# Kernel optimization log

Measured on AMD Instinct MI355X. Metric: run time of the kernel, lower is better.

The kernel has to match this reference:

```python
import jax, jax.numpy as jnp
import numpy as np

C = 512       # out_channels
RATIO = 2
K = C // RATIO          # init_channels = 256
NEW = K * (RATIO - 1)   # new_channels = 256
H = W = 160
EPS = 1e-5


def _conv(x, w, pad, groups=1):
    return jax.lax.conv_general_dilated(
        x, w, (1, 1), [(pad, pad), (pad, pad)],
        dimension_numbers=("NCHW", "OIHW", "NCHW"),
        feature_group_count=groups)


def _bn(x, g, b, m, v):
    scale = (g / jnp.sqrt(v + EPS))[None, :, None, None]
    return (x - m[None, :, None, None]) * scale + b[None, :, None, None]


def setup_inputs() -> dict:
    key = jax.random.key(0)
    ks = jax.random.split(key, 16)
    s = 0.05
    return {
        "x": jax.random.normal(ks[0], (1, C, H, W), jnp.float32),
        "w_fc1": jax.random.normal(ks[1], (K, C), jnp.float32) * s,
        "w_fc2": jax.random.normal(ks[2], (C, K), jnp.float32) * s,
        "w_cheap": jax.random.normal(ks[3], (NEW, 1, 3, 3), jnp.float32) * s,  # depthwise, groups=K
        "bn1_g": jnp.ones((NEW,), jnp.float32),
        "bn1_b": jnp.zeros((NEW,), jnp.float32),
        "bn1_m": jax.random.normal(ks[4], (NEW,), jnp.float32) * s,
        "bn1_v": jax.random.uniform(ks[5], (NEW,), jnp.float32, 0.5, 1.5),
        "w_dc1": jax.random.normal(ks[6], (C, 2 * C, 1, 1), jnp.float32) * s,
        "b_dc1": jax.random.normal(ks[7], (C,), jnp.float32) * s,
        "bn2_g": jnp.ones((C,), jnp.float32),
        "bn2_b": jnp.zeros((C,), jnp.float32),
        "bn2_m": jax.random.normal(ks[8], (C,), jnp.float32) * s,
        "bn2_v": jax.random.uniform(ks[9], (C,), jnp.float32, 0.5, 1.5),
        "w_dc2": jax.random.normal(ks[10], (C, C, 3, 3), jnp.float32) * s,
        "b_dc2": jax.random.normal(ks[11], (C,), jnp.float32) * s,
    }


def reference(x, w_fc1, w_fc2, w_cheap, bn1_g, bn1_b, bn1_m, bn1_v,
              w_dc1, b_dc1, bn2_g, bn2_b, bn2_m, bn2_v, w_dc2, b_dc2):
    # ---- channel attention (CBAM-style shared MLP over avg+max pool) ----
    avg = x.mean(axis=(2, 3))                      # [1, C]
    mx = x.max(axis=(2, 3))                        # [1, C]
    mlp = lambda p: jax.nn.relu(p @ w_fc1.T) @ w_fc2.T
    scales = jax.nn.sigmoid(mlp(avg) + mlp(mx))    # [1, C]
    # ---- sort-based top-K channel select, kept in channel-index order ----
    # torch: sort desc, drop channels ranked >= K via boolean mask (mask is in
    # channel-index order), equivalent to gathering sorted top-K indices.
    _, top_idx = jax.lax.top_k(scales[0], K)
    idx = jnp.sort(top_idx)
    x1 = x[:, idx]                                 # [1, K, H, W]
    # ---- cheap operation: depthwise 3x3 + BN + ReLU ----
    x2 = jax.nn.relu(_bn(_conv(x1, w_cheap, 1, groups=K), bn1_g, bn1_b, bn1_m, bn1_v))
    # ---- concat [x*scales, x1, x2] -> 2C channels ----
    cat = jnp.concatenate([x * scales[:, :, None, None], x1, x2], axis=1)
    # ---- down_channel: 1x1 conv + BN + 3x3 conv + ReLU ----
    h = _conv(cat, w_dc1, 0) + b_dc1[None, :, None, None]
    h = _bn(h, bn2_g, bn2_b, bn2_m, bn2_v)
    h = _conv(h, w_dc2, 1) + b_dc2[None, :, None, None]
    return jax.nn.relu(h)
```

## Files before the change

kernel.cpp:

```cpp
#include <hip/hip_runtime.h>
#include <math.h>

#define C 512
#define K 256
#define HW 160
#define NPIX (HW*HW)
#define PW 162
#define EPS 1e-5f

typedef __attribute__((ext_vector_type(8))) short s16x8;
typedef __attribute__((ext_vector_type(16))) float f32x16;

__device__ __forceinline__ unsigned short f2bf(float f) {
    unsigned int u = __float_as_uint(f);
    u += 0x7fffu + ((u >> 16) & 1u);
    return (unsigned short)(u >> 16);
}

__device__ __forceinline__ void ldg_lds16(const void* g, void* l) {
    __builtin_amdgcn_global_load_lds((const __attribute__((address_space(1))) unsigned int*)g,
                                     (__attribute__((address_space(3))) unsigned int*)l, 16, 0, 0);
}

#define WAIT_VM0()   asm volatile("s_waitcnt vmcnt(0)" ::: "memory")
#define WAIT_VM14()  asm volatile("s_waitcnt vmcnt(14)" ::: "memory")
#define WAIT_VM23()  asm volatile("s_waitcnt vmcnt(23)" ::: "memory")

__global__ void reduce_kernel(const float* __restrict__ x,
                              float* __restrict__ avg, float* __restrict__ mx) {
    int c = blockIdx.x;
    const float4* xc = (const float4*)(x + (size_t)c * NPIX);
    float s = 0.f, m = -INFINITY;
    for (int p = threadIdx.x; p < NPIX / 4; p += 256) {
        float4 v = xc[p];
        s += v.x + v.y + v.z + v.w;
        m = fmaxf(m, fmaxf(fmaxf(v.x, v.y), fmaxf(v.z, v.w)));
    }
    __shared__ float ss[256], sm[256];
    ss[threadIdx.x] = s; sm[threadIdx.x] = m;
    __syncthreads();
    for (int o = 128; o > 0; o >>= 1) {
        if (threadIdx.x < o) {
            ss[threadIdx.x] += ss[threadIdx.x + o];
            sm[threadIdx.x] = fmaxf(sm[threadIdx.x], sm[threadIdx.x + o]);
        }
        __syncthreads();
    }
    if (threadIdx.x == 0) {
        avg[c] = ss[0] / (float)NPIX;
        mx[c]  = sm[0];
    }
}

__global__ void mlp_select_kernel(const float* __restrict__ avg,
                                  const float* __restrict__ mx,
                                  const float* __restrict__ w_fc1,
                                  const float* __restrict__ w_fc2,
                                  float* __restrict__ scales_out,
                                  int* __restrict__ idx,
                                  int* __restrict__ pos) {
    __shared__ float s_avg[C], s_mx[C], s_h[K], s_scales[C];
    __shared__ int s_sel[C];
    int t = threadIdx.x;
    s_avg[t] = avg[t];
    s_mx[t]  = mx[t];
    __syncthreads();
    if (t < K) {
        float ha = 0.f, hm = 0.f;
        const float4* wr = (const float4*)(w_fc1 + (size_t)t * C);
        for (int c = 0; c < C / 4; c++) {
            float4 w = wr[c];
            ha += s_avg[4*c]*w.x + s_avg[4*c+1]*w.y + s_avg[4*c+2]*w.z + s_avg[4*c+3]*w.w;
            hm += s_mx[4*c]*w.x + s_mx[4*c+1]*w.y + s_mx[4*c+2]*w.z + s_mx[4*c+3]*w.w;
        }
        s_h[t] = fmaxf(ha, 0.f) + fmaxf(hm, 0.f);
    }
    __syncthreads();
    {
        float o = 0.f;
        const float4* wr = (const float4*)(w_fc2 + (size_t)t * K);
        for (int k = 0; k < K / 4; k++) {
            float4 w = wr[k];
            o += s_h[4*k]*w.x + s_h[4*k+1]*w.y + s_h[4*k+2]*w.z + s_h[4*k+3]*w.w;
        }
        float sc = 1.f / (1.f + expf(-o));
        s_scales[t] = sc;
        scales_out[t] = sc;
    }
    __syncthreads();
    {
        float v = s_scales[t];
        int rank = 0;
        for (int i = 0; i < C; i++) {
            float u = s_scales[i];
            rank += (u > v) || (u == v && i < t);
        }
        s_sel[t] = (rank < K) ? 1 : 0;
    }
    __syncthreads();
    {
        int p = 0;
        for (int i = 0; i < t; i++) p += s_sel[i];
        if (s_sel[t]) { idx[p] = t; pos[t] = p; }
        else pos[t] = -1;
    }
}

__global__ void prep_kernel(const float* __restrict__ w_dc2, unsigned short* __restrict__ w3,
                            const float* __restrict__ w_dc1, const float* __restrict__ scales,
                            const int* __restrict__ pos, unsigned short* __restrict__ wA,
                            unsigned short* __restrict__ hpad,
                            const float* __restrict__ b_dc1,
                            const float* __restrict__ g2, const float* __restrict__ b2,
                            const float* __restrict__ m2, const float* __restrict__ v2,
                            float* __restrict__ scale2, float* __restrict__ shift2) {
    __shared__ unsigned short lw[4608];
    int b = blockIdx.x;
    if (b < 512) {
        int co = b;
        const float* src = w_dc2 + (size_t)co * 4608;
        for (int u = threadIdx.x; u < 4608; u += 256)
            lw[u] = f2bf(src[u]);
        __syncthreads();
        for (int u = threadIdx.x; u < 4608; u += 256) {
            int t = u >> 9, ci = u & 511;
            w3[((size_t)t * 512 + co) * 512 + ci] = lw[ci * 9 + t];
        }
    } else if (b < 1024) {
        int co = b - 512;
        const float* wr = w_dc1 + (size_t)co * 1024;
        for (int c = threadIdx.x; c < 768; c += 256) {
            float v;
            if (c < 512) {
                v = wr[c] * scales[c];
                int pp = pos[c];
                if (pp >= 0) v += wr[512 + pp];
            } else {
                v = wr[768 + (c - 512)];
            }
            wA[(size_t)co * 768 + c] = f2bf(v);
        }
    } else if (b < 1185) {
        int t = (b - 1024) * 256 + threadIdx.x;
        int pix = t >> 6;
        int p;
        if (pix < 162)      p = pix;
        else if (pix < 324) p = 161 * PW + (pix - 162);
        else {
            int r = pix - 324;
            p = (1 + (r >> 1)) * PW + ((r & 1) ? 161 : 0);
        }
        *(uint4*)&hpad[(size_t)p * 512 + (t & 63) * 8] = make_uint4(0u, 0u, 0u, 0u);
    } else {
        for (int c = threadIdx.x; c < C; c += 256) {
            float s = g2[c] * rsqrtf(v2[c] + EPS);
            scale2[c] = s;
            shift2[c] = (b_dc1[c] - m2[c]) * s + b2[c];
        }
    }
}

__global__ void dw_t_kernel(const float* __restrict__ x,
                            const int* __restrict__ idx,
                            const float* __restrict__ wch,
                            const float* __restrict__ g1, const float* __restrict__ b1,
                            const float* __restrict__ m1, const float* __restrict__ v1,
                            unsigned short* __restrict__ xcat) {
    __shared__ float tile[32][33];
    int tx = threadIdx.x & 31, ty = threadIdx.x >> 5;
    int pbase = blockIdx.x * 32, kbase = blockIdx.y * 32;
    int y = pbase / HW, x0 = pbase % HW;
    int px = x0 + tx;
#pragma unroll
    for (int jj = 0; jj < 4; jj++) {
        int k = kbase + ty + jj * 8;
        int c = idx[k];
        const float* xc = x + (size_t)c * NPIX;
        const float* wk = wch + k * 9;
        float acc = 0.f;
#pragma unroll
        for (int dy = 0; dy < 3; dy++) {
            int yy = y + dy - 1;
            if (yy < 0 || yy >= HW) continue;
#pragma unroll
            for (int dx = 0; dx < 3; dx++) {
                int xv = px + dx - 1;
                if (xv < 0 || xv >= HW) continue;
                acc += xc[yy * HW + xv] * wk[dy * 3 + dx];
            }
        }
        float s = g1[k] * rsqrtf(v1[k] + EPS);
        tile[ty + jj * 8][tx] = fmaxf((acc - m1[k]) * s + b1[k], 0.f);
    }
    __syncthreads();
#pragma unroll
    for (int jj = 0; jj < 4; jj++) {
        int p = pbase + ty + jj * 8;
        xcat[(size_t)p * 768 + 512 + kbase + tx] = f2bf(tile[tx][ty + jj * 8]);
    }
}

__global__ void transpose_kernel(const float* __restrict__ x,
                                 unsigned short* __restrict__ xcat) {
    __shared__ float tile[32][33];
    int tx = threadIdx.x & 31, ty = threadIdx.x >> 5;
    int pbase = blockIdx.x * 32, cbase = blockIdx.y * 32;
#pragma unroll
    for (int j = 0; j < 4; j++) {
        int c = cbase + ty + j * 8;
        tile[ty + j * 8][tx] = x[(size_t)c * NPIX + pbase + tx];
    }
    __syncthreads();
#pragma unroll
    for (int j = 0; j < 4; j++) {
        int p = pbase + ty + j * 8;
        xcat[(size_t)p * 768 + cbase + tx] = f2bf(tile[tx][ty + j * 8]);
    }
}

__global__ __launch_bounds__(64, 1) void conv1_mfma(const unsigned short* __restrict__ xcat,
        const unsigned short* __restrict__ wA,
        const float* __restrict__ scale2, const float* __restrict__ shift2,
        unsigned short* __restrict__ hpad) {
    __shared__ unsigned short Al[3][640 * 8];
    __shared__ unsigned short Bl[3][256 * 8];
    int y = blockIdx.x, co0 = blockIdx.y * 64;
    int lane = threadIdx.x;
    int l31 = lane & 31, q = lane >> 5;
    f32x16 acc[5][2] = {};

    int aoff[10], boff[4];
#pragma unroll
    for (int r = 0; r < 10; r++) {
        int g = r * 64 + lane;
        int px = g >> 2, jg = (g & 3) ^ ((px >> 1) & 3);
        aoff[r] = px * 768 + jg * 8;
    }
#pragma unroll
    for (int r = 0; r < 4; r++) {
        int g = r * 64 + lane;
        int co = g >> 2, jg = (g & 3) ^ ((co >> 1) & 3);
        boff[r] = co * 768 + jg * 8;
    }
    int raoff[2];
#pragma unroll
    for (int s = 0; s < 2; s++)
        raoff[s] = l31 * 64 + (((s * 2 + q) ^ ((l31 >> 1) & 3)) << 4);
    const unsigned short* arow = xcat + (size_t)y * HW * 768;
    const unsigned short* brow = wA + (size_t)co0 * 768;

    auto stage = [&](int ph, int buf) {
        int kc = ph * 32;
        unsigned short* An = Al[buf];
        unsigned short* Bn = Bl[buf];
#pragma unroll
        for (int r = 0; r < 10; r++) ldg_lds16(arow + kc + aoff[r], &An[r * 512]);
#pragma unroll
        for (int r = 0; r < 4; r++)  ldg_lds16(brow + kc + boff[r], &Bn[r * 512]);
    };

    stage(0, 0);
    stage(1, 1);
    for (int ph = 0; ph < 24; ph++) {
        const unsigned short* Ar = Al[ph % 3];
        const unsigned short* Br = Bl[ph % 3];
        if (ph == 23) { WAIT_VM0(); } else { WAIT_VM14(); }
#pragma unroll
        for (int s = 0; s < 2; s++) {
            s16x8 af[5], bf[2];
#pragma unroll
            for (int i = 0; i < 5; i++)
                af[i] = *(const s16x8*)((const char*)Ar + i * 2048 + raoff[s]);
#pragma unroll
            for (int j = 0; j < 2; j++)
                bf[j] = *(const s16x8*)((const char*)Br + j * 2048 + raoff[s]);
            if (s == 0 && ph < 22) stage(ph + 2, (ph + 2) % 3);
#pragma unroll
            for (int i = 0; i < 5; i++)
#pragma unroll
                for (int j = 0; j < 2; j++)
                    acc[i][j] = __builtin_amdgcn_mfma_f32_32x32x16_bf16(af[i], bf[j], acc[i][j], 0, 0, 0);
        }
    }
#pragma unroll
    for (int j = 0; j < 2; j++) {
        int co = co0 + j * 32 + l31;
        float s2 = scale2[co], sh = shift2[co];
#pragma unroll
        for (int i = 0; i < 5; i++) {
#pragma unroll
            for (int rg = 0; rg < 4; rg++) {
#pragma unroll
                for (int t = 0; t < 4; t++) {
                    int px = i * 32 + t + rg * 8 + q * 4;
                    size_t pp = (size_t)(y + 1) * PW + px + 1;
                    hpad[pp * 512 + co] = f2bf(acc[i][j][rg * 4 + t] * s2 + sh);
                }
            }
        }
    }
}

__global__ __launch_bounds__(64, 1) void conv3_mfma(const unsigned short* __restrict__ hpad,
        const unsigned short* __restrict__ w3,
        const float* __restrict__ bias, float* __restrict__ out) {
    __shared__ unsigned short Al[3][648 * 8];
    __shared__ unsigned short Bl[3][768 * 8];
    int y = blockIdx.x, co0 = blockIdx.y * 64;
    int lane = threadIdx.x;
    int l31 = lane & 31, q = lane >> 5;
    f32x16 acc[5][2] = {};

    int aoff[11], boff[12];
#pragma unroll
    for (int r = 0; r < 11; r++) {
        int g = r * 64 + lane;
        int px = g >> 2, jg = (g & 3) ^ ((px >> 1) & 3);
        aoff[r] = px * 512 + jg * 8;
    }
#pragma unroll
    for (int r = 0; r < 12; r++) {
        int g = r * 64 + lane;
        int tt = g >> 8, co = (g >> 2) & 63, jg = (g & 3) ^ ((co >> 1) & 3);
        boff[r] = (tt * 512 + co) * 512 + jg * 8;
    }
    int raoff[3][2], rboff[2];
#pragma unroll
    for (int dx = 0; dx < 3; dx++)
#pragma unroll
        for (int s = 0; s < 2; s++) {
            int m = l31 + dx;
            raoff[dx][s] = m * 64 + ((((s * 2 + q)) ^ ((m >> 1) & 3)) << 4);
        }
#pragma unroll
    for (int s = 0; s < 2; s++)
        rboff[s] = l31 * 64 + (((s * 2 + q) ^ ((l31 >> 1) & 3)) << 4);

    auto stage = [&](int ph, int buf) {
        int dy = ph >> 4, kc = (ph & 15) * 32;
        const unsigned short* ab = hpad + ((size_t)(y + dy) * PW) * 512 + kc;
        unsigned short* An = Al[buf];
#pragma unroll
        for (int r = 0; r < 10; r++) ldg_lds16(ab + aoff[r], &An[r * 512]);
        if (lane < 8)                ldg_lds16(ab + aoff[10], &An[10 * 512]);
        const unsigned short* bb = w3 + ((size_t)(dy * 3) * 512 + co0) * 512 + kc;
        unsigned short* Bn = Bl[buf];
#pragma unroll
        for (int r = 0; r < 12; r++) ldg_lds16(bb + boff[r], &Bn[r * 512]);
    };

    stage(0, 0);
    stage(1, 1);
    for (int ph = 0; ph < 48; ph++) {
        const unsigned short* Ar = Al[ph % 3];
        const unsigned short* Br = Bl[ph % 3];
        if (ph == 47) { WAIT_VM0(); } else { WAIT_VM23(); }
#pragma unroll
        for (int dx = 0; dx < 3; dx++) {
            s16x8 af[5][2], bf[2][2];
#pragma unroll
            for (int s = 0; s < 2; s++) {
#pragma unroll
                for (int i = 0; i < 5; i++)
                    af[i][s] = *(const s16x8*)((const char*)Ar + i * 2048 + raoff[dx][s]);
#pragma unroll
                for (int j = 0; j < 2; j++)
                    bf[j][s] = *(const s16x8*)((const char*)Br + dx * 4096 + j * 2048 + rboff[s]);
            }
            if (dx == 0 && ph < 46) stage(ph + 2, (ph + 2) % 3);
#pragma unroll
            for (int s = 0; s < 2; s++)
#pragma unroll
                for (int i = 0; i < 5; i++)
#pragma unroll
                    for (int j = 0; j < 2; j++)
                        acc[i][j] = __builtin_amdgcn_mfma_f32_32x32x16_bf16(af[i][s], bf[j][s], acc[i][j], 0, 0, 0);
        }
    }
#pragma unroll
    for (int j = 0; j < 2; j++) {
        int co = co0 + j * 32 + l31;
        float b = bias[co];
        float* op = out + (size_t)co * NPIX + y * HW;
#pragma unroll
        for (int i = 0; i < 5; i++) {
#pragma unroll
            for (int rg = 0; rg < 4; rg++) {
                int px = i * 32 + rg * 8 + q * 4;
                float4 v;
                v.x = fmaxf(acc[i][j][rg * 4 + 0] + b, 0.f);
                v.y = fmaxf(acc[i][j][rg * 4 + 1] + b, 0.f);
                v.z = fmaxf(acc[i][j][rg * 4 + 2] + b, 0.f);
                v.w = fmaxf(acc[i][j][rg * 4 + 3] + b, 0.f);
                *(float4*)&op[px] = v;
            }
        }
    }
}

extern "C" void kernel_launch(void* const* d_in, const int* in_sizes, int n_in,
                              void* d_out, int out_size, void* d_ws, size_t ws_size,
                              hipStream_t stream) {
    const float* x      = (const float*)d_in[0];
    const float* w_fc1  = (const float*)d_in[1];
    const float* w_fc2  = (const float*)d_in[2];
    const float* w_ch   = (const float*)d_in[3];
    const float* bn1_g  = (const float*)d_in[4];
    const float* bn1_b  = (const float*)d_in[5];
    const float* bn1_m  = (const float*)d_in[6];
    const float* bn1_v  = (const float*)d_in[7];
    const float* w_dc1  = (const float*)d_in[8];
    const float* b_dc1  = (const float*)d_in[9];
    const float* bn2_g  = (const float*)d_in[10];
    const float* bn2_b  = (const float*)d_in[11];
    const float* bn2_m  = (const float*)d_in[12];
    const float* bn2_v  = (const float*)d_in[13];
    const float* w_dc2  = (const float*)d_in[14];
    const float* b_dc2  = (const float*)d_in[15];
    float* out = (float*)d_out;

    char* ws = (char*)d_ws;
    float* avg    = (float*)(ws + 0);
    float* mx     = (float*)(ws + 2048);
    float* scales = (float*)(ws + 4096);
    int*   idx    = (int*)  (ws + 6144);
    int*   pos    = (int*)  (ws + 7168);
    float* scale2 = (float*)(ws + 9216);
    float* shift2 = (float*)(ws + 11264);
    unsigned short* wA   = (unsigned short*)(ws + 16384);
    unsigned short* w3   = (unsigned short*)(ws + 802816);
    unsigned short* xcat = (unsigned short*)(ws + 31735808);
    unsigned short* hpad = (unsigned short*)(ws + 71057408);

    reduce_kernel<<<C, 256, 0, stream>>>(x, avg, mx);
    mlp_select_kernel<<<1, C, 0, stream>>>(avg, mx, w_fc1, w_fc2, scales, idx, pos);
    prep_kernel<<<1186, 256, 0, stream>>>(w_dc2, w3, w_dc1, scales, pos, wA, hpad,
                                          b_dc1, bn2_g, bn2_b, bn2_m, bn2_v, scale2, shift2);
    dw_t_kernel<<<dim3(800, 8), 256, 0, stream>>>(x, idx, w_ch, bn1_g, bn1_b, bn1_m, bn1_v, xcat);
    transpose_kernel<<<dim3(800, 16), 256, 0, stream>>>(x, xcat);
    conv1_mfma<<<dim3(HW, 8), 64, 0, stream>>>(xcat, wA, scale2, shift2, hpad);
    conv3_mfma<<<dim3(HW, 8), 64, 0, stream>>>(hpad, w3, b_dc2, out);
}
```

Measured before the change: 531.6 us.

## Pre-swizzle conv weights into MFMA fragment order and load B directly to registers

The prep kernel now writes the 1x1 and 3x3 conv weights in bf16, laid out in the exact per-lane MFMA fragment order. Both MFMA conv kernels then load the B operand straight from global memory into registers instead of staging it through LDS. This frees LDS and removes the B-side LDS traffic and waits. The conv3 A pipeline drops from triple to double buffering with a full vmcnt(0) wait each phase, which exposes more global-load latency. The weight prep also changes from a transpose through shared memory to strided gathers.

```diff
diff --git a/kernel.cpp b/kernel.cpp
--- a/kernel.cpp
+++ b/kernel.cpp
@@ -23,8 +23,7 @@
 }
 
 #define WAIT_VM0()   asm volatile("s_waitcnt vmcnt(0)" ::: "memory")
-#define WAIT_VM14()  asm volatile("s_waitcnt vmcnt(14)" ::: "memory")
-#define WAIT_VM23()  asm volatile("s_waitcnt vmcnt(23)" ::: "memory")
+#define WAIT_VM10()  asm volatile("s_waitcnt vmcnt(10)" ::: "memory")
 
 __global__ void reduce_kernel(const float* __restrict__ x,
                               float* __restrict__ avg, float* __restrict__ mx) {
@@ -106,30 +105,38 @@
     }
 }
 
-__global__ void prep_kernel(const float* __restrict__ w_dc2, unsigned short* __restrict__ w3,
+__global__ void prep_kernel(const float* __restrict__ w_dc2, unsigned short* __restrict__ w3f,
                             const float* __restrict__ w_dc1, const float* __restrict__ scales,
-                            const int* __restrict__ pos, unsigned short* __restrict__ wA,
+                            const int* __restrict__ pos, unsigned short* __restrict__ wAf,
                             unsigned short* __restrict__ hpad,
                             const float* __restrict__ b_dc1,
                             const float* __restrict__ g2, const float* __restrict__ b2,
                             const float* __restrict__ m2, const float* __restrict__ v2,
                             float* __restrict__ scale2, float* __restrict__ shift2) {
-    __shared__ unsigned short lw[4608];
     int b = blockIdx.x;
-    if (b < 512) {
-        int co = b;
-        const float* src = w_dc2 + (size_t)co * 4608;
-        for (int u = threadIdx.x; u < 4608; u += 256)
-            lw[u] = f2bf(src[u]);
-        __syncthreads();
-        for (int u = threadIdx.x; u < 4608; u += 256) {
-            int t = u >> 9, ci = u & 511;
-            w3[((size_t)t * 512 + co) * 512 + ci] = lw[ci * 9 + t];
-        }
-    } else if (b < 1024) {
-        int co = b - 512;
-        const float* wr = w_dc1 + (size_t)co * 1024;
-        for (int c = threadIdx.x; c < 768; c += 256) {
+    if (b < 384) {
+        int g = b / 48, ph = b % 48;
+        int dy = ph >> 4, kc = ph & 15;
+        for (int u = threadIdx.x; u < 6144; u += 256) {
+            int chunk = u >> 9;
+            int dx = chunk >> 2, j = (chunk >> 1) & 1, s = chunk & 1;
+            int r = u & 511, lane = r >> 3, e = r & 7;
+            int co = g * 64 + j * 32 + (lane & 31);
+            int qq = lane >> 5;
+            int ci = kc * 32 + (s * 2 + qq) * 8 + e;
+            w3f[(size_t)b * 6144 + u] = f2bf(w_dc2[((size_t)co * 512 + ci) * 9 + dy * 3 + dx]);
+        }
+    } else if (b < 576) {
+        int bb = b - 384;
+        int g = bb / 24, ph = bb % 24;
+        for (int u = threadIdx.x; u < 2048; u += 256) {
+            int chunk = u >> 9;
+            int j = chunk >> 1, s = chunk & 1;
+            int r = u & 511, lane = r >> 3, e = r & 7;
+            int co = g * 64 + j * 32 + (lane & 31);
+            int qq = lane >> 5;
+            int c = ph * 32 + (s * 2 + qq) * 8 + e;
+            const float* wr = w_dc1 + (size_t)co * 1024;
             float v;
             if (c < 512) {
                 v = wr[c] * scales[c];
@@ -138,10 +145,10 @@
             } else {
                 v = wr[768 + (c - 512)];
             }
-            wA[(size_t)co * 768 + c] = f2bf(v);
-        }
-    } else if (b < 1185) {
-        int t = (b - 1024) * 256 + threadIdx.x;
+            wAf[(size_t)bb * 2048 + u] = f2bf(v);
+        }
+    } else if (b < 737) {
+        int t = (b - 576) * 256 + threadIdx.x;
         int pix = t >> 6;
         int p;
         if (pix < 162)      p = pix;
@@ -219,68 +226,62 @@
 }
 
 __global__ __launch_bounds__(64, 1) void conv1_mfma(const unsigned short* __restrict__ xcat,
-        const unsigned short* __restrict__ wA,
+        const unsigned short* __restrict__ wAf,
         const float* __restrict__ scale2, const float* __restrict__ shift2,
         unsigned short* __restrict__ hpad) {
     __shared__ unsigned short Al[3][640 * 8];
-    __shared__ unsigned short Bl[3][256 * 8];
-    int y = blockIdx.x, co0 = blockIdx.y * 64;
+    int y = blockIdx.x, g = blockIdx.y, co0 = g * 64;
     int lane = threadIdx.x;
     int l31 = lane & 31, q = lane >> 5;
     f32x16 acc[5][2] = {};
 
-    int aoff[10], boff[4];
+    int aoff[10];
 #pragma unroll
     for (int r = 0; r < 10; r++) {
-        int g = r * 64 + lane;
-        int px = g >> 2, jg = (g & 3) ^ ((px >> 1) & 3);
+        int gg = r * 64 + lane;
+        int px = gg >> 2, jg = (gg & 3) ^ ((px >> 1) & 3);
         aoff[r] = px * 768 + jg * 8;
-    }
-#pragma unroll
-    for (int r = 0; r < 4; r++) {
-        int g = r * 64 + lane;
-        int co = g >> 2, jg = (g & 3) ^ ((co >> 1) & 3);
-        boff[r] = co * 768 + jg * 8;
     }
     int raoff[2];
 #pragma unroll
     for (int s = 0; s < 2; s++)
         raoff[s] = l31 * 64 + (((s * 2 + q) ^ ((l31 >> 1) & 3)) << 4);
     const unsigned short* arow = xcat + (size_t)y * HW * 768;
-    const unsigned short* brow = wA + (size_t)co0 * 768;
-
-    auto stage = [&](int ph, int buf) {
+    const s16x8* bbase = (const s16x8*)wAf + ((size_t)g * 24) * 256 + lane;
+
+    auto stageA = [&](int ph, int buf) {
         int kc = ph * 32;
         unsigned short* An = Al[buf];
-        unsigned short* Bn = Bl[buf];
 #pragma unroll
         for (int r = 0; r < 10; r++) ldg_lds16(arow + kc + aoff[r], &An[r * 512]);
-#pragma unroll
-        for (int r = 0; r < 4; r++)  ldg_lds16(brow + kc + boff[r], &Bn[r * 512]);
     };
 
-    stage(0, 0);
-    stage(1, 1);
+    stageA(0, 0);
+    stageA(1, 1);
     for (int ph = 0; ph < 24; ph++) {
         const unsigned short* Ar = Al[ph % 3];
-        const unsigned short* Br = Bl[ph % 3];
-        if (ph == 23) { WAIT_VM0(); } else { WAIT_VM14(); }
-#pragma unroll
-        for (int s = 0; s < 2; s++) {
-            s16x8 af[5], bf[2];
+        if (ph == 23) { WAIT_VM0(); } else { WAIT_VM10(); }
+        const s16x8* bp = bbase + (size_t)ph * 256;
+        s16x8 bf[2][2];
+#pragma unroll
+        for (int j = 0; j < 2; j++)
+#pragma unroll
+            for (int s = 0; s < 2; s++)
+                bf[j][s] = bp[(j * 2 + s) * 64];
+        s16x8 af[5][2];
+#pragma unroll
+        for (int s = 0; s < 2; s++)
 #pragma unroll
             for (int i = 0; i < 5; i++)
-                af[i] = *(const s16x8*)((const char*)Ar + i * 2048 + raoff[s]);
-#pragma unroll
-            for (int j = 0; j < 2; j++)
-                bf[j] = *(const s16x8*)((const char*)Br + j * 2048 + raoff[s]);
-            if (s == 0 && ph < 22) stage(ph + 2, (ph + 2) % 3);
+                af[i][s] = *(const s16x8*)((const char*)Ar + i * 2048 + raoff[s]);
+        if (ph < 22) stageA(ph + 2, (ph + 2) % 3);
+#pragma unroll
+        for (int s = 0; s < 2; s++)
 #pragma unroll
             for (int i = 0; i < 5; i++)
 #pragma unroll
                 for (int j = 0; j < 2; j++)
-                    acc[i][j] = __builtin_amdgcn_mfma_f32_32x32x16_bf16(af[i], bf[j], acc[i][j], 0, 0, 0);
-        }
+                    acc[i][j] = __builtin_amdgcn_mfma_f32_32x32x16_bf16(af[i][s], bf[j][s], acc[i][j], 0, 0, 0);
     }
 #pragma unroll
     for (int j = 0; j < 2; j++) {
@@ -302,29 +303,22 @@
 }
 
 __global__ __launch_bounds__(64, 1) void conv3_mfma(const unsigned short* __restrict__ hpad,
-        const unsigned short* __restrict__ w3,
+        const unsigned short* __restrict__ w3f,
         const float* __restrict__ bias, float* __restrict__ out) {
-    __shared__ unsigned short Al[3][648 * 8];
-    __shared__ unsigned short Bl[3][768 * 8];
-    int y = blockIdx.x, co0 = blockIdx.y * 64;
+    __shared__ unsigned short Al[2][648 * 8];
+    int y = blockIdx.x, g = blockIdx.y, co0 = g * 64;
     int lane = threadIdx.x;
     int l31 = lane & 31, q = lane >> 5;
     f32x16 acc[5][2] = {};
 
-    int aoff[11], boff[12];
+    int aoff[11];
 #pragma unroll
     for (int r = 0; r < 11; r++) {
-        int g = r * 64 + lane;
-        int px = g >> 2, jg = (g & 3) ^ ((px >> 1) & 3);
+        int gg = r * 64 + lane;
+        int px = gg >> 2, jg = (gg & 3) ^ ((px >> 1) & 3);
         aoff[r] = px * 512 + jg * 8;
     }
-#pragma unroll
-    for (int r = 0; r < 12; r++) {
-        int g = r * 64 + lane;
-        int tt = g >> 8, co = (g >> 2) & 63, jg = (g & 3) ^ ((co >> 1) & 3);
-        boff[r] = (tt * 512 + co) * 512 + jg * 8;
-    }
-    int raoff[3][2], rboff[2];
+    int raoff[3][2];
 #pragma unroll
     for (int dx = 0; dx < 3; dx++)
 #pragma unroll
@@ -332,49 +326,46 @@
             int m = l31 + dx;
             raoff[dx][s] = m * 64 + ((((s * 2 + q)) ^ ((m >> 1) & 3)) << 4);
         }
-#pragma unroll
-    for (int s = 0; s < 2; s++)
-        rboff[s] = l31 * 64 + (((s * 2 + q) ^ ((l31 >> 1) & 3)) << 4);
-
-    auto stage = [&](int ph, int buf) {
+    const s16x8* bbase = (const s16x8*)w3f + ((size_t)g * 48) * 768 + lane;
+
+    auto stageA = [&](int ph, int buf) {
         int dy = ph >> 4, kc = (ph & 15) * 32;
         const unsigned short* ab = hpad + ((size_t)(y + dy) * PW) * 512 + kc;
         unsigned short* An = Al[buf];
 #pragma unroll
         for (int r = 0; r < 10; r++) ldg_lds16(ab + aoff[r], &An[r * 512]);
         if (lane < 8)                ldg_lds16(ab + aoff[10], &An[10 * 512]);
-        const unsigned short* bb = w3 + ((size_t)(dy * 3) * 512 + co0) * 512 + kc;
-        unsigned short* Bn = Bl[buf];
-#pragma unroll
-        for (int r = 0; r < 12; r++) ldg_lds16(bb + boff[r], &Bn[r * 512]);
     };
 
-    stage(0, 0);
-    stage(1, 1);
+    stageA(0, 0);
     for (int ph = 0; ph < 48; ph++) {
-        const unsigned short* Ar = Al[ph % 3];
-        const unsigned short* Br = Bl[ph % 3];
-        if (ph == 47) { WAIT_VM0(); } else { WAIT_VM23(); }
+        const unsigned short* Ar = Al[ph & 1];
+        WAIT_VM0();
+        const s16x8* bp = bbase + (size_t)ph * 768;
+        s16x8 bf[3][2][2];
+#pragma unroll
+        for (int dx = 0; dx < 3; dx++)
+#pragma unroll
+            for (int j = 0; j < 2; j++)
+#pragma unroll
+                for (int s = 0; s < 2; s++)
+                    bf[dx][j][s] = bp[(dx * 4 + j * 2 + s) * 64];
 #pragma unroll
         for (int dx = 0; dx < 3; dx++) {
-            s16x8 af[5][2], bf[2][2];
-#pragma unroll
-            for (int s = 0; s < 2; s++) {
+            s16x8 af[5][2];
+#pragma unroll
+            for (int s = 0; s < 2; s++)
 #pragma unroll
                 for (int i = 0; i < 5; i++)
                     af[i][s] = *(const s16x8*)((const char*)Ar + i * 2048 + raoff[dx][s]);
-#pragma unroll
-                for (int j = 0; j < 2; j++)
-                    bf[j][s] = *(const s16x8*)((const char*)Br + dx * 4096 + j * 2048 + rboff[s]);
-            }
-            if (dx == 0 && ph < 46) stage(ph + 2, (ph + 2) % 3);
+            if (dx == 0 && ph < 47) stageA(ph + 1, (ph + 1) & 1);
 #pragma unroll
             for (int s = 0; s < 2; s++)
 #pragma unroll
                 for (int i = 0; i < 5; i++)
 #pragma unroll
                     for (int j = 0; j < 2; j++)
-                        acc[i][j] = __builtin_amdgcn_mfma_f32_32x32x16_bf16(af[i][s], bf[j][s], acc[i][j], 0, 0, 0);
+                        acc[i][j] = __builtin_amdgcn_mfma_f32_32x32x16_bf16(af[i][s], bf[dx][j][s], acc[i][j], 0, 0, 0);
         }
     }
 #pragma unroll
@@ -427,17 +418,17 @@
     int*   pos    = (int*)  (ws + 7168);
     float* scale2 = (float*)(ws + 9216);
     float* shift2 = (float*)(ws + 11264);
-    unsigned short* wA   = (unsigned short*)(ws + 16384);
-    unsigned short* w3   = (unsigned short*)(ws + 802816);
+    unsigned short* wAf  = (unsigned short*)(ws + 16384);
+    unsigned short* w3f  = (unsigned short*)(ws + 802816);
     unsigned short* xcat = (unsigned short*)(ws + 31735808);
     unsigned short* hpad = (unsigned short*)(ws + 71057408);
 
     reduce_kernel<<<C, 256, 0, stream>>>(x, avg, mx);
     mlp_select_kernel<<<1, C, 0, stream>>>(avg, mx, w_fc1, w_fc2, scales, idx, pos);
-    prep_kernel<<<1186, 256, 0, stream>>>(w_dc2, w3, w_dc1, scales, pos, wA, hpad,
-                                          b_dc1, bn2_g, bn2_b, bn2_m, bn2_v, scale2, shift2);
+    prep_kernel<<<738, 256, 0, stream>>>(w_dc2, w3f, w_dc1, scales, pos, wAf, hpad,
+                                         b_dc1, bn2_g, bn2_b, bn2_m, bn2_v, scale2, shift2);
     dw_t_kernel<<<dim3(800, 8), 256, 0, stream>>>(x, idx, w_ch, bn1_g, bn1_b, bn1_m, bn1_v, xcat);
     transpose_kernel<<<dim3(800, 16), 256, 0, stream>>>(x, xcat);
-    conv1_mfma<<<dim3(HW, 8), 64, 0, stream>>>(xcat, wA, scale2, shift2, hpad);
-    conv3_mfma<<<dim3(HW, 8), 64, 0, stream>>>(hpad, w3, b_dc2, out);
-}
+    conv1_mfma<<<dim3(HW, 8), 64, 0, stream>>>(xcat, wAf, scale2, shift2, hpad);
+    conv3_mfma<<<dim3(HW, 8), 64, 0, stream>>>(hpad, w3f, b_dc2, out);
+}
```

Result: faster. 476.2 us (-10.4%).

## Split channel-attention MLP into parallel kernels and double-buffer conv pipelines

Applied to the files above, without the earlier changes.

The single-block MLP+select kernel becomes three kernels: fc1 and fc2 each spread across many wavefronts with shuffle reductions, followed by a small select kernel. Both MFMA conv kernels move from a 3-stage LDS ring with partial vmcnt waits to 2-stage double buffering with a full wait before issuing the next stage. This cuts serial latency in the tiny MLP and lowers LDS use, but it shortens prefetch depth, so global loads may overlap less with MFMA work in the dominant conv kernels.

```diff
diff --git a/kernel.cpp b/kernel.cpp
--- a/kernel.cpp
+++ b/kernel.cpp
@@ -23,8 +23,6 @@
 }
 
 #define WAIT_VM0()   asm volatile("s_waitcnt vmcnt(0)" ::: "memory")
-#define WAIT_VM14()  asm volatile("s_waitcnt vmcnt(14)" ::: "memory")
-#define WAIT_VM23()  asm volatile("s_waitcnt vmcnt(23)" ::: "memory")
 
 __global__ void reduce_kernel(const float* __restrict__ x,
                               float* __restrict__ avg, float* __restrict__ mx) {
@@ -52,41 +50,39 @@
     }
 }
 
-__global__ void mlp_select_kernel(const float* __restrict__ avg,
-                                  const float* __restrict__ mx,
-                                  const float* __restrict__ w_fc1,
-                                  const float* __restrict__ w_fc2,
-                                  float* __restrict__ scales_out,
-                                  int* __restrict__ idx,
-                                  int* __restrict__ pos) {
-    __shared__ float s_avg[C], s_mx[C], s_h[K], s_scales[C];
+__global__ void fc1_kernel(const float* __restrict__ avg, const float* __restrict__ mx,
+                           const float* __restrict__ w_fc1, float* __restrict__ h) {
+    int t = blockIdx.x, lane = threadIdx.x;
+    const float* wr = w_fc1 + (size_t)t * C;
+    float pa = 0.f, pm = 0.f;
+    for (int c = lane; c < C; c += 64) {
+        float w = wr[c];
+        pa += avg[c] * w;
+        pm += mx[c] * w;
+    }
+    for (int o = 32; o > 0; o >>= 1) {
+        pa += __shfl_down(pa, o);
+        pm += __shfl_down(pm, o);
+    }
+    if (lane == 0) h[t] = fmaxf(pa, 0.f) + fmaxf(pm, 0.f);
+}
+
+__global__ void fc2_kernel(const float* __restrict__ h, const float* __restrict__ w_fc2,
+                           float* __restrict__ scales) {
+    int c = blockIdx.x, lane = threadIdx.x;
+    const float* wr = w_fc2 + (size_t)c * K;
+    float o = 0.f;
+    for (int k = lane; k < K; k += 64) o += h[k] * wr[k];
+    for (int s = 32; s > 0; s >>= 1) o += __shfl_down(o, s);
+    if (lane == 0) scales[c] = 1.f / (1.f + expf(-o));
+}
+
+__global__ void select_kernel(const float* __restrict__ scales,
+                              int* __restrict__ idx, int* __restrict__ pos) {
+    __shared__ float s_scales[C];
     __shared__ int s_sel[C];
     int t = threadIdx.x;
-    s_avg[t] = avg[t];
-    s_mx[t]  = mx[t];
-    __syncthreads();
-    if (t < K) {
-        float ha = 0.f, hm = 0.f;
-        const float4* wr = (const float4*)(w_fc1 + (size_t)t * C);
-        for (int c = 0; c < C / 4; c++) {
-            float4 w = wr[c];
-            ha += s_avg[4*c]*w.x + s_avg[4*c+1]*w.y + s_avg[4*c+2]*w.z + s_avg[4*c+3]*w.w;
-            hm += s_mx[4*c]*w.x + s_mx[4*c+1]*w.y + s_mx[4*c+2]*w.z + s_mx[4*c+3]*w.w;
-        }
-        s_h[t] = fmaxf(ha, 0.f) + fmaxf(hm, 0.f);
-    }
-    __syncthreads();
-    {
-        float o = 0.f;
-        const float4* wr = (const float4*)(w_fc2 + (size_t)t * K);
-        for (int k = 0; k < K / 4; k++) {
-            float4 w = wr[k];
-            o += s_h[4*k]*w.x + s_h[4*k+1]*w.y + s_h[4*k+2]*w.z + s_h[4*k+3]*w.w;
-        }
-        float sc = 1.f / (1.f + expf(-o));
-        s_scales[t] = sc;
-        scales_out[t] = sc;
-    }
+    s_scales[t] = scales[t];
     __syncthreads();
     {
         float v = s_scales[t];
@@ -222,8 +218,8 @@
         const unsigned short* __restrict__ wA,
         const float* __restrict__ scale2, const float* __restrict__ shift2,
         unsigned short* __restrict__ hpad) {
-    __shared__ unsigned short Al[3][640 * 8];
-    __shared__ unsigned short Bl[3][256 * 8];
+    __shared__ unsigned short Al[2][640 * 8];
+    __shared__ unsigned short Bl[2][256 * 8];
     int y = blockIdx.x, co0 = blockIdx.y * 64;
     int lane = threadIdx.x;
     int l31 = lane & 31, q = lane >> 5;
@@ -260,27 +256,28 @@
     };
 
     stage(0, 0);
-    stage(1, 1);
     for (int ph = 0; ph < 24; ph++) {
-        const unsigned short* Ar = Al[ph % 3];
-        const unsigned short* Br = Bl[ph % 3];
-        if (ph == 23) { WAIT_VM0(); } else { WAIT_VM14(); }
+        const unsigned short* Ar = Al[ph & 1];
+        const unsigned short* Br = Bl[ph & 1];
+        WAIT_VM0();
+        if (ph < 23) stage(ph + 1, (ph + 1) & 1);
+        s16x8 af[5][2], bf[2][2];
 #pragma unroll
         for (int s = 0; s < 2; s++) {
-            s16x8 af[5], bf[2];
 #pragma unroll
             for (int i = 0; i < 5; i++)
-                af[i] = *(const s16x8*)((const char*)Ar + i * 2048 + raoff[s]);
+                af[i][s] = *(const s16x8*)((const char*)Ar + i * 2048 + raoff[s]);
 #pragma unroll
             for (int j = 0; j < 2; j++)
-                bf[j] = *(const s16x8*)((const char*)Br + j * 2048 + raoff[s]);
-            if (s == 0 && ph < 22) stage(ph + 2, (ph + 2) % 3);
+                bf[j][s] = *(const s16x8*)((const char*)Br + j * 2048 + raoff[s]);
+        }
+#pragma unroll
+        for (int s = 0; s < 2; s++)
 #pragma unroll
             for (int i = 0; i < 5; i++)
 #pragma unroll
                 for (int j = 0; j < 2; j++)
-                    acc[i][j] = __builtin_amdgcn_mfma_f32_32x32x16_bf16(af[i], bf[j], acc[i][j], 0, 0, 0);
-        }
+                    acc[i][j] = __builtin_amdgcn_mfma_f32_32x32x16_bf16(af[i][s], bf[j][s], acc[i][j], 0, 0, 0);
     }
 #pragma unroll
     for (int j = 0; j < 2; j++) {
@@ -304,8 +301,8 @@
 __global__ __launch_bounds__(64, 1) void conv3_mfma(const unsigned short* __restrict__ hpad,
         const unsigned short* __restrict__ w3,
         const float* __restrict__ bias, float* __restrict__ out) {
-    __shared__ unsigned short Al[3][648 * 8];
-    __shared__ unsigned short Bl[3][768 * 8];
+    __shared__ unsigned short Al[2][648 * 8];
+    __shared__ unsigned short Bl[2][768 * 8];
     int y = blockIdx.x, co0 = blockIdx.y * 64;
     int lane = threadIdx.x;
     int l31 = lane & 31, q = lane >> 5;
@@ -350,11 +347,11 @@
     };
 
     stage(0, 0);
-    stage(1, 1);
     for (int ph = 0; ph < 48; ph++) {
-        const unsigned short* Ar = Al[ph % 3];
-        const unsigned short* Br = Bl[ph % 3];
-        if (ph == 47) { WAIT_VM0(); } else { WAIT_VM23(); }
+        const unsigned short* Ar = Al[ph & 1];
+        const unsigned short* Br = Bl[ph & 1];
+        WAIT_VM0();
+        if (ph < 47) stage(ph + 1, (ph + 1) & 1);
 #pragma unroll
         for (int dx = 0; dx < 3; dx++) {
             s16x8 af[5][2], bf[2][2];
@@ -367,7 +364,6 @@
                 for (int j = 0; j < 2; j++)
                     bf[j][s] = *(const s16x8*)((const char*)Br + dx * 4096 + j * 2048 + rboff[s]);
             }
-            if (dx == 0 && ph < 46) stage(ph + 2, (ph + 2) % 3);
 #pragma unroll
             for (int s = 0; s < 2; s++)
 #pragma unroll
@@ -427,13 +423,16 @@
     int*   pos    = (int*)  (ws + 7168);
     float* scale2 = (float*)(ws + 9216);
     float* shift2 = (float*)(ws + 11264);
+    float* hbuf   = (float*)(ws + 13312);
     unsigned short* wA   = (unsigned short*)(ws + 16384);
     unsigned short* w3   = (unsigned short*)(ws + 802816);
     unsigned short* xcat = (unsigned short*)(ws + 31735808);
     unsigned short* hpad = (unsigned short*)(ws + 71057408);
 
     reduce_kernel<<<C, 256, 0, stream>>>(x, avg, mx);
-    mlp_select_kernel<<<1, C, 0, stream>>>(avg, mx, w_fc1, w_fc2, scales, idx, pos);
+    fc1_kernel<<<K, 64, 0, stream>>>(avg, mx, w_fc1, hbuf);
+    fc2_kernel<<<C, 64, 0, stream>>>(hbuf, w_fc2, scales);
+    select_kernel<<<1, C, 0, stream>>>(scales, idx, pos);
     prep_kernel<<<1186, 256, 0, stream>>>(w_dc2, w3, w_dc1, scales, pos, wA, hpad,
                                           b_dc1, bn2_g, bn2_b, bn2_m, bn2_v, scale2, shift2);
     dw_t_kernel<<<dim3(800, 8), 256, 0, stream>>>(x, idx, w_ch, bn1_g, bn1_b, bn1_m, bn1_v, xcat);
```

New measurement: 475.8 us. -10.5%, faster.
